# Kernel optimization log

Measured on AMD Instinct MI355X. Metric: run time of the kernel, lower is better.

Reference implementation:

```python
import jax, jax.numpy as jnp
import numpy as np

N_NODES = 10000
N_EDGES = 640000
D_IN, D_HID, D_OUT = 128, 128, 64


def setup_inputs() -> dict:
    key = jax.random.key(0)
    ks = jax.random.split(key, 12)
    inp = {
        "inputs": jax.random.normal(ks[0], (N_NODES, D_IN), dtype=jnp.float32),
        "W_self0": jax.random.normal(ks[1], (D_IN, D_HID), dtype=jnp.float32) / np.sqrt(D_IN),
        "W_neigh0": jax.random.normal(ks[2], (D_IN, D_HID), dtype=jnp.float32) / np.sqrt(D_IN),
        "b0": jnp.zeros((D_HID,), dtype=jnp.float32),
        "W_self1": jax.random.normal(ks[3], (D_HID, D_HID), dtype=jnp.float32) / np.sqrt(D_HID),
        "W_neigh1": jax.random.normal(ks[4], (D_HID, D_HID), dtype=jnp.float32) / np.sqrt(D_HID),
        "b1": jnp.zeros((D_HID,), dtype=jnp.float32),
        "W_self2": jax.random.normal(ks[5], (D_HID, D_OUT), dtype=jnp.float32) / np.sqrt(D_HID),
        "W_neigh2": jax.random.normal(ks[6], (D_HID, D_OUT), dtype=jnp.float32) / np.sqrt(D_HID),
        "b2": jnp.zeros((D_OUT,), dtype=jnp.float32),
        "edge_src": jax.random.randint(ks[7], (N_EDGES,), 0, N_NODES, dtype=jnp.int32),
        "edge_dst": jax.random.randint(ks[8], (N_EDGES,), 0, N_NODES, dtype=jnp.int32),
    }
    return inp


def _sage_conv(h, W_self, W_neigh, b, edge_src, edge_dst):
    # mean aggregation: mean of source-node features over incoming edges at dst
    gathered = h[edge_src]                                   # [E, d] irregular gather
    agg = jax.ops.segment_sum(gathered, edge_dst, num_segments=N_NODES)  # [N, d]
    deg = jax.ops.segment_sum(jnp.ones((edge_dst.shape[0],), h.dtype), edge_dst,
                              num_segments=N_NODES)          # [N]
    h_neigh = agg / jnp.maximum(deg, 1.0)[:, None]
    return h @ W_self + h_neigh @ W_neigh + b


def reference(inputs, W_self0, W_neigh0, b0, W_self1, W_neigh1, b1,
              W_self2, W_neigh2, b2, edge_src, edge_dst):
    # dropout p=0.0 -> identity
    h = _sage_conv(inputs, W_self0, W_neigh0, b0, edge_src, edge_dst)
    h = jax.nn.relu(h)
    h = _sage_conv(h, W_self1, W_neigh1, b1, edge_src, edge_dst)
    h = jax.nn.relu(h)
    h = _sage_conv(h, W_self2, W_neigh2, b2, edge_src, edge_dst)
    return h
```

## Files before the change

kernel.cpp:

```cpp
#include <hip/hip_runtime.h>


#define NN 10000
#define NE 640000
#define NBINS 313
#define NBLKA 250
#define CHUNK 2560
#define CAP 3072
#define SORT_CAP 4096

typedef __attribute__((ext_vector_type(8))) short s8v;
typedef __attribute__((ext_vector_type(4))) float f4v;

__device__ __forceinline__ ushort f2bf(float f) {
    unsigned u = __float_as_uint(f);
    return (ushort)((u + 0x7FFFu + ((u >> 16) & 1u)) >> 16);
}
__device__ __forceinline__ unsigned pack2(float a, float b) {
    return (unsigned)f2bf(a) | ((unsigned)f2bf(b) << 16);
}
__device__ __forceinline__ float bf_lo(unsigned u) { return __uint_as_float(u << 16); }
__device__ __forceinline__ float bf_hi(unsigned u) { return __uint_as_float(u & 0xFFFF0000u); }


__global__ void prep_k(const float* __restrict__ x, ushort* __restrict__ xb,
                       const float* __restrict__ Ws0, const float* __restrict__ Wn0,
                       const float* __restrict__ Ws1, const float* __restrict__ Wn1,
                       const float* __restrict__ Ws2, const float* __restrict__ Wn2,
                       ushort* __restrict__ wt, int* __restrict__ bincnt) {
    __shared__ ushort ps[128 * 128];
    int blk = blockIdx.x, tid = threadIdx.x;
    if (blk < 64) {
        const float4* xv = (const float4*)x;
        uint2* xo = (uint2*)xb;
        for (int i = tid; i < 5000; i += 256) {
            int idx = blk * 5000 + i;
            float4 v = xv[idx];
            xo[idx] = make_uint2(pack2(v.x, v.y), pack2(v.z, v.w));
        }
    } else if (blk < 70) {
        int m = blk - 64;
        const float* W = (m == 0) ? Ws0 : (m == 1) ? Wn0 : (m == 2) ? Ws1
                       : (m == 3) ? Wn1 : (m == 4) ? Ws2 : Wn2;
        int MC = (m < 4) ? 128 : 64;
        ushort* dst = wt + ((m < 4) ? m * 16384 : 65536 + (m - 4) * 8192);
        int tot = 128 * MC;
        for (int idx = tid; idx < tot; idx += 256) {
            int k = (MC == 128) ? (idx >> 7) : (idx >> 6);
            int n = (MC == 128) ? (idx & 127) : (idx & 63);
            ps[n * 128 + k] = f2bf(W[idx]);
        }
        __syncthreads();
        for (int idx = tid; idx < tot; idx += 256)
            dst[idx] = ps[idx];
    } else {
        for (int i = tid; i < NBINS; i += 256) bincnt[i] = 0;
    }
}


__device__ void scatter_body(const int* __restrict__ src, const int* __restrict__ dst,
                             int* __restrict__ bincnt, unsigned* __restrict__ tmp2,
                             int blk, int* smem) {
    int* h = smem;
    int* cur = smem + NBINS;
    int tid = threadIdx.x;
    for (int i = tid; i < NBINS; i += 256) h[i] = 0;
    __syncthreads();
    int base = blk * CHUNK;
    for (int i = tid; i < CHUNK; i += 256)
        atomicAdd(&h[dst[base + i] >> 5], 1);
    __syncthreads();
    for (int bin = tid; bin < NBINS; bin += 256) {
        int c = h[bin];
        int off = c ? atomicAdd(&bincnt[bin], c) : 0;
        cur[bin] = bin * CAP + off;
    }
    __syncthreads();
    for (int i = tid; i < CHUNK; i += 256) {
        int d = dst[base + i], s = src[base + i];
        int bin = d >> 5;
        int pos = atomicAdd(&cur[bin], 1);
        if (pos < bin * CAP + CAP)
            tmp2[pos] = ((unsigned)s << 5) | (unsigned)(d & 31);
    }
}

__device__ void dense0_body(const ushort* __restrict__ xb, const ushort* __restrict__ wt,
                            const float* __restrict__ b0,
                            float* __restrict__ hs, ushort* __restrict__ hn, int dblk) {
    int l = threadIdx.x & 63, w = threadIdx.x >> 6;
    int mloc = l & 15, quad = l >> 4;
    int row_base = dblk * 32 + (w & 1) * 16;
    int colh = w >> 1;
    int arow = row_base + mloc;
    int arow_c = (arow < NN) ? arow : (NN - 1);
    const ushort* wsT = wt;
    const ushort* wnT = wt + 16384;
    f4v accS[4], accN[4];
#pragma unroll
    for (int nt = 0; nt < 4; ++nt) { accS[nt] = (f4v){0,0,0,0}; accN[nt] = (f4v){0,0,0,0}; }
#pragma unroll
    for (int ks = 0; ks < 4; ++ks) {
        int kb = ks * 32 + quad * 8;
        s8v a = *(const s8v*)(xb + (size_t)arow_c * 128 + kb);
#pragma unroll
        for (int nt = 0; nt < 4; ++nt) {
            int n = colh * 64 + nt * 16 + mloc;
            s8v bs = *(const s8v*)(wsT + n * 128 + kb);
            s8v bn = *(const s8v*)(wnT + n * 128 + kb);
            accS[nt] = __builtin_amdgcn_mfma_f32_16x16x32_bf16(a, bs, accS[nt], 0, 0, 0);
            accN[nt] = __builtin_amdgcn_mfma_f32_16x16x32_bf16(a, bn, accN[nt], 0, 0, 0);
        }
    }
#pragma unroll
    for (int nt = 0; nt < 4; ++nt) {
        int col = colh * 64 + nt * 16 + mloc;
        float bv = b0[col];
#pragma unroll
        for (int r = 0; r < 4; ++r) {
            int row = row_base + quad * 4 + r;
            if (row < NN) {
                hs[(size_t)row * 128 + col] = accS[nt][r] + bv;
                hn[(size_t)row * 128 + col] = f2bf(accN[nt][r]);
            }
        }
    }
}

__global__ void scatdense_k(const int* __restrict__ esrc, const int* __restrict__ edst,
                            int* __restrict__ bincnt, unsigned* __restrict__ tmp2,
                            const ushort* __restrict__ xb, const ushort* __restrict__ wt,
                            const float* __restrict__ b0,
                            float* __restrict__ hs, ushort* __restrict__ hn) {
    __shared__ int smem[2 * NBINS];
    int blk = blockIdx.x;
    if (blk < NBLKA)
        scatter_body(esrc, edst, bincnt, tmp2, blk, smem);
    else
        dense0_body(xb, wt, b0, hs, hn, blk - NBLKA);
}


__global__ void sort_k(const unsigned* __restrict__ tmp2, const int* __restrict__ bincnt,
                       int* __restrict__ offs, int* __restrict__ ends,
                       int* __restrict__ ssrc) {
    __shared__ int stage[SORT_CAP];
    __shared__ int cnt32[32];
    __shared__ int cur32[32];
    int b = blockIdx.x, tid = threadIdx.x;
    int beg = b * CAP;
    int cnt = bincnt[b];
    if (cnt > CAP) cnt = CAP;
    if (tid < 32) cnt32[tid] = 0;
    __syncthreads();
    for (int i = tid; i < cnt; i += 256)
        atomicAdd(&cnt32[tmp2[beg + i] & 31], 1);
    __syncthreads();
    if (tid == 0) {
        int run = 0;
        for (int i = 0; i < 32; ++i) {
            int node = b * 32 + i;
            if (node < NN) { offs[node] = beg + run; ends[node] = beg + run + cnt32[i]; }
            cur32[i] = run;
            run += cnt32[i];
        }
    }
    __syncthreads();
    for (int i = tid; i < cnt; i += 256) {
        unsigned q = tmp2[beg + i];
        int pos = atomicAdd(&cur32[q & 31], 1);
        stage[pos] = (int)(q >> 5);
    }
    __syncthreads();
    for (int i = tid; i < cnt; i += 256)
        ssrc[beg + i] = stage[i];
}


template <int MOUT>
__global__ void agg_dense_k(const float* __restrict__ hs_in, const ushort* __restrict__ hn_in,
                            const int* __restrict__ offs, const int* __restrict__ ends,
                            const int* __restrict__ ssrc,
                            const ushort* __restrict__ wsT, const ushort* __restrict__ wnT,
                            const float* __restrict__ bias,
                            float* __restrict__ hs_out, ushort* __restrict__ hn_out) {
    __shared__ ushort hrow[16 * 136];
    int tid = threadIdx.x;
    int node_loc = tid >> 4, t = tid & 15;
    int node = blockIdx.x * 16 + node_loc;
    int beg = offs[node], end = ends[node];
    const uint4* hn4 = (const uint4*)hn_in;
    float a0 = 0, a1 = 0, a2 = 0, a3 = 0, a4 = 0, a5 = 0, a6 = 0, a7 = 0;
    int e = beg;
    for (; e + 8 <= end; e += 8) {
        int s0 = ssrc[e], s1 = ssrc[e + 1], s2 = ssrc[e + 2], s3 = ssrc[e + 3];
        int s4 = ssrc[e + 4], s5 = ssrc[e + 5], s6 = ssrc[e + 6], s7 = ssrc[e + 7];
        uint4 v0 = hn4[(size_t)s0 * 16 + t];
        uint4 v1 = hn4[(size_t)s1 * 16 + t];
        uint4 v2 = hn4[(size_t)s2 * 16 + t];
        uint4 v3 = hn4[(size_t)s3 * 16 + t];
        uint4 v4 = hn4[(size_t)s4 * 16 + t];
        uint4 v5 = hn4[(size_t)s5 * 16 + t];
        uint4 v6 = hn4[(size_t)s6 * 16 + t];
        uint4 v7 = hn4[(size_t)s7 * 16 + t];
        a0 += bf_lo(v0.x) + bf_lo(v1.x) + bf_lo(v2.x) + bf_lo(v3.x)
            + bf_lo(v4.x) + bf_lo(v5.x) + bf_lo(v6.x) + bf_lo(v7.x);
        a1 += bf_hi(v0.x) + bf_hi(v1.x) + bf_hi(v2.x) + bf_hi(v3.x)
            + bf_hi(v4.x) + bf_hi(v5.x) + bf_hi(v6.x) + bf_hi(v7.x);
        a2 += bf_lo(v0.y) + bf_lo(v1.y) + bf_lo(v2.y) + bf_lo(v3.y)
            + bf_lo(v4.y) + bf_lo(v5.y) + bf_lo(v6.y) + bf_lo(v7.y);
        a3 += bf_hi(v0.y) + bf_hi(v1.y) + bf_hi(v2.y) + bf_hi(v3.y)
            + bf_hi(v4.y) + bf_hi(v5.y) + bf_hi(v6.y) + bf_hi(v7.y);
        a4 += bf_lo(v0.z) + bf_lo(v1.z) + bf_lo(v2.z) + bf_lo(v3.z)
            + bf_lo(v4.z) + bf_lo(v5.z) + bf_lo(v6.z) + bf_lo(v7.z);
        a5 += bf_hi(v0.z) + bf_hi(v1.z) + bf_hi(v2.z) + bf_hi(v3.z)
            + bf_hi(v4.z) + bf_hi(v5.z) + bf_hi(v6.z) + bf_hi(v7.z);
        a6 += bf_lo(v0.w) + bf_lo(v1.w) + bf_lo(v2.w) + bf_lo(v3.w)
            + bf_lo(v4.w) + bf_lo(v5.w) + bf_lo(v6.w) + bf_lo(v7.w);
        a7 += bf_hi(v0.w) + bf_hi(v1.w) + bf_hi(v2.w) + bf_hi(v3.w)
            + bf_hi(v4.w) + bf_hi(v5.w) + bf_hi(v6.w) + bf_hi(v7.w);
    }
    for (; e < end; ++e) {
        uint4 v = hn4[(size_t)ssrc[e] * 16 + t];
        a0 += bf_lo(v.x); a1 += bf_hi(v.x); a2 += bf_lo(v.y); a3 += bf_hi(v.y);
        a4 += bf_lo(v.z); a5 += bf_hi(v.z); a6 += bf_lo(v.w); a7 += bf_hi(v.w);
    }
    int deg = end - beg;
    float sc = 1.0f / (float)(deg > 0 ? deg : 1);
    float4 h4a = ((const float4*)hs_in)[(size_t)node * 32 + 2 * t];
    float4 h4b = ((const float4*)hs_in)[(size_t)node * 32 + 2 * t + 1];
    float r0 = fmaxf(h4a.x + a0 * sc, 0.f), r1 = fmaxf(h4a.y + a1 * sc, 0.f);
    float r2 = fmaxf(h4a.z + a2 * sc, 0.f), r3 = fmaxf(h4a.w + a3 * sc, 0.f);
    float r4 = fmaxf(h4b.x + a4 * sc, 0.f), r5 = fmaxf(h4b.y + a5 * sc, 0.f);
    float r6 = fmaxf(h4b.z + a6 * sc, 0.f), r7 = fmaxf(h4b.w + a7 * sc, 0.f);
    *(uint4*)(hrow + node_loc * 136 + t * 8) =
        make_uint4(pack2(r0, r1), pack2(r2, r3), pack2(r4, r5), pack2(r6, r7));
    __syncthreads();

    int l = tid & 63, w = tid >> 6;
    int mloc = l & 15, quad = l >> 4;
    constexpr int NTPW = MOUT / 64;
    f4v accS[NTPW], accN[NTPW];
#pragma unroll
    for (int nt = 0; nt < NTPW; ++nt) { accS[nt] = (f4v){0,0,0,0}; accN[nt] = (f4v){0,0,0,0}; }
#pragma unroll
    for (int ks = 0; ks < 4; ++ks) {
        int kb = ks * 32 + quad * 8;
        s8v a = *(const s8v*)(hrow + mloc * 136 + kb);
#pragma unroll
        for (int nt = 0; nt < NTPW; ++nt) {
            int n = (w * NTPW + nt) * 16 + mloc;
            s8v bs = *(const s8v*)(wsT + n * 128 + kb);
            s8v bn = *(const s8v*)(wnT + n * 128 + kb);
            accS[nt] = __builtin_amdgcn_mfma_f32_16x16x32_bf16(a, bs, accS[nt], 0, 0, 0);
            accN[nt] = __builtin_amdgcn_mfma_f32_16x16x32_bf16(a, bn, accN[nt], 0, 0, 0);
        }
    }
#pragma unroll
    for (int nt = 0; nt < NTPW; ++nt) {
        int col = (w * NTPW + nt) * 16 + mloc;
        float bv = bias[col];
#pragma unroll
        for (int r = 0; r < 4; ++r) {
            int row = blockIdx.x * 16 + quad * 4 + r;
            hs_out[(size_t)row * MOUT + col] = accS[nt][r] + bv;
            hn_out[(size_t)row * MOUT + col] = f2bf(accN[nt][r]);
        }
    }
}


__global__ void agg_out_k(const float* __restrict__ hs_in, const ushort* __restrict__ hn_in,
                          const int* __restrict__ offs, const int* __restrict__ ends,
                          const int* __restrict__ ssrc, float* __restrict__ out) {
    int tid = threadIdx.x;
    int node = blockIdx.x * 32 + (tid >> 3);
    int t = tid & 7;
    if (node >= NN) return;
    int beg = offs[node], end = ends[node];
    const uint4* hn4 = (const uint4*)hn_in;
    float a0 = 0, a1 = 0, a2 = 0, a3 = 0, a4 = 0, a5 = 0, a6 = 0, a7 = 0;
    int e = beg;
    for (; e + 8 <= end; e += 8) {
        int s0 = ssrc[e], s1 = ssrc[e + 1], s2 = ssrc[e + 2], s3 = ssrc[e + 3];
        int s4 = ssrc[e + 4], s5 = ssrc[e + 5], s6 = ssrc[e + 6], s7 = ssrc[e + 7];
        uint4 v0 = hn4[(size_t)s0 * 8 + t];
        uint4 v1 = hn4[(size_t)s1 * 8 + t];
        uint4 v2 = hn4[(size_t)s2 * 8 + t];
        uint4 v3 = hn4[(size_t)s3 * 8 + t];
        uint4 v4 = hn4[(size_t)s4 * 8 + t];
        uint4 v5 = hn4[(size_t)s5 * 8 + t];
        uint4 v6 = hn4[(size_t)s6 * 8 + t];
        uint4 v7 = hn4[(size_t)s7 * 8 + t];
        a0 += bf_lo(v0.x) + bf_lo(v1.x) + bf_lo(v2.x) + bf_lo(v3.x)
            + bf_lo(v4.x) + bf_lo(v5.x) + bf_lo(v6.x) + bf_lo(v7.x);
        a1 += bf_hi(v0.x) + bf_hi(v1.x) + bf_hi(v2.x) + bf_hi(v3.x)
            + bf_hi(v4.x) + bf_hi(v5.x) + bf_hi(v6.x) + bf_hi(v7.x);
        a2 += bf_lo(v0.y) + bf_lo(v1.y) + bf_lo(v2.y) + bf_lo(v3.y)
            + bf_lo(v4.y) + bf_lo(v5.y) + bf_lo(v6.y) + bf_lo(v7.y);
        a3 += bf_hi(v0.y) + bf_hi(v1.y) + bf_hi(v2.y) + bf_hi(v3.y)
            + bf_hi(v4.y) + bf_hi(v5.y) + bf_hi(v6.y) + bf_hi(v7.y);
        a4 += bf_lo(v0.z) + bf_lo(v1.z) + bf_lo(v2.z) + bf_lo(v3.z)
            + bf_lo(v4.z) + bf_lo(v5.z) + bf_lo(v6.z) + bf_lo(v7.z);
        a5 += bf_hi(v0.z) + bf_hi(v1.z) + bf_hi(v2.z) + bf_hi(v3.z)
            + bf_hi(v4.z) + bf_hi(v5.z) + bf_hi(v6.z) + bf_hi(v7.z);
        a6 += bf_lo(v0.w) + bf_lo(v1.w) + bf_lo(v2.w) + bf_lo(v3.w)
            + bf_lo(v4.w) + bf_lo(v5.w) + bf_lo(v6.w) + bf_lo(v7.w);
        a7 += bf_hi(v0.w) + bf_hi(v1.w) + bf_hi(v2.w) + bf_hi(v3.w)
            + bf_hi(v4.w) + bf_hi(v5.w) + bf_hi(v6.w) + bf_hi(v7.w);
    }
    for (; e < end; ++e) {
        uint4 v = hn4[(size_t)ssrc[e] * 8 + t];
        a0 += bf_lo(v.x); a1 += bf_hi(v.x); a2 += bf_lo(v.y); a3 += bf_hi(v.y);
        a4 += bf_lo(v.z); a5 += bf_hi(v.z); a6 += bf_lo(v.w); a7 += bf_hi(v.w);
    }
    int deg = end - beg;
    float sc = 1.0f / (float)(deg > 0 ? deg : 1);
    float4 h4a = ((const float4*)hs_in)[(size_t)node * 16 + 2 * t];
    float4 h4b = ((const float4*)hs_in)[(size_t)node * 16 + 2 * t + 1];
    ((float4*)out)[(size_t)node * 16 + 2 * t] =
        make_float4(h4a.x + a0 * sc, h4a.y + a1 * sc, h4a.z + a2 * sc, h4a.w + a3 * sc);
    ((float4*)out)[(size_t)node * 16 + 2 * t + 1] =
        make_float4(h4b.x + a4 * sc, h4b.y + a5 * sc, h4b.z + a6 * sc, h4b.w + a7 * sc);
}


extern "C" void kernel_launch(void* const* d_in, const int* in_sizes, int n_in,
                              void* d_out, int out_size, void* d_ws, size_t ws_size,
                              hipStream_t stream) {
    const float* x   = (const float*)d_in[0];
    const float* Ws0 = (const float*)d_in[1];
    const float* Wn0 = (const float*)d_in[2];
    const float* b0  = (const float*)d_in[3];
    const float* Ws1 = (const float*)d_in[4];
    const float* Wn1 = (const float*)d_in[5];
    const float* b1  = (const float*)d_in[6];
    const float* Ws2 = (const float*)d_in[7];
    const float* Wn2 = (const float*)d_in[8];
    const float* b2  = (const float*)d_in[9];
    const int* esrc  = (const int*)d_in[10];
    const int* edst  = (const int*)d_in[11];
    float* out = (float*)d_out;

    float*  hsA = (float*)d_ws;
    float*  hsB = hsA + (size_t)NN * 128;
    ushort* hnA = (ushort*)(hsB + (size_t)NN * 128);
    ushort* hnB = hnA + (size_t)NN * 128;
    ushort* xb  = hnB + (size_t)NN * 128;
    ushort* wt  = xb + (size_t)NN * 128;
    unsigned* tmp2 = (unsigned*)(wt + 81920);
    int* ssrc = (int*)(tmp2 + (size_t)NBINS * CAP);
    int* offs = ssrc + (size_t)NBINS * CAP;
    int* ends = offs + NN;
    int* bincnt = ends + NN;

    prep_k<<<71, 256, 0, stream>>>(x, xb, Ws0, Wn0, Ws1, Wn1, Ws2, Wn2, wt, bincnt);
    scatdense_k<<<NBLKA + 313, 256, 0, stream>>>(esrc, edst, bincnt, tmp2,
                                                 xb, wt, b0, hsA, hnA);
    sort_k<<<NBINS, 256, 0, stream>>>(tmp2, bincnt, offs, ends, ssrc);
    agg_dense_k<128><<<NN / 16, 256, 0, stream>>>(hsA, hnA, offs, ends, ssrc,
                                                  wt + 32768, wt + 49152, b1, hsB, hnB);
    agg_dense_k<64><<<NN / 16, 256, 0, stream>>>(hsB, hnB, offs, ends, ssrc,
                                                 wt + 65536, wt + 73728, b2, hsA, hnA);
    agg_out_k<<<(NN + 31) / 32, 256, 0, stream>>>(hsA, hnA, offs, ends, ssrc, out);
}
```

Before: 169.2 us.

## Fuse input bf16 conversion into dense0 and move weight transposes into scatter kernel

Drops the separate pass that converts the node features to bf16; dense0 now reads fp32 rows directly and converts them in registers. The prep kernel shrinks to two blocks that only transpose the layer-0 weights, while the layer-1/2 weight transposes run as extra blocks of the scatter/dense kernel. The scatter pass now caches the packed edge words in shared memory so src/dst are read from global only once. This removes a full write and read of the bf16 feature buffer and shortens the prep launch, at the cost of a larger shared-memory footprint per block, which may lower occupancy, and of each dense0 block repeating the conversions.

Result: no change. 167.2 us (-1.2%).

```diff
diff --git a/kernel.cpp b/kernel.cpp
--- a/kernel.cpp
+++ b/kernel.cpp
@@ -22,39 +22,30 @@
 __device__ __forceinline__ float bf_lo(unsigned u) { return __uint_as_float(u << 16); }
 __device__ __forceinline__ float bf_hi(unsigned u) { return __uint_as_float(u & 0xFFFF0000u); }
 
-
-__global__ void prep_k(const float* __restrict__ x, ushort* __restrict__ xb,
-                       const float* __restrict__ Ws0, const float* __restrict__ Wn0,
-                       const float* __restrict__ Ws1, const float* __restrict__ Wn1,
-                       const float* __restrict__ Ws2, const float* __restrict__ Wn2,
+__device__ void wtrans_body(const float* __restrict__ W, ushort* __restrict__ dst,
+                            int MC, ushort* ps) {
+    int tid = threadIdx.x;
+    int tot = 128 * MC;
+    for (int idx = tid; idx < tot; idx += 256) {
+        int k = (MC == 128) ? (idx >> 7) : (idx >> 6);
+        int n = (MC == 128) ? (idx & 127) : (idx & 63);
+        ps[n * 128 + k] = f2bf(W[idx]);
+    }
+    __syncthreads();
+    for (int idx = tid; idx < tot; idx += 256)
+        dst[idx] = ps[idx];
+}
+
+
+__global__ void prep_k(const float* __restrict__ Ws0, const float* __restrict__ Wn0,
                        ushort* __restrict__ wt, int* __restrict__ bincnt) {
     __shared__ ushort ps[128 * 128];
     int blk = blockIdx.x, tid = threadIdx.x;
-    if (blk < 64) {
-        const float4* xv = (const float4*)x;
-        uint2* xo = (uint2*)xb;
-        for (int i = tid; i < 5000; i += 256) {
-            int idx = blk * 5000 + i;
-            float4 v = xv[idx];
-            xo[idx] = make_uint2(pack2(v.x, v.y), pack2(v.z, v.w));
-        }
-    } else if (blk < 70) {
-        int m = blk - 64;
-        const float* W = (m == 0) ? Ws0 : (m == 1) ? Wn0 : (m == 2) ? Ws1
-                       : (m == 3) ? Wn1 : (m == 4) ? Ws2 : Wn2;
-        int MC = (m < 4) ? 128 : 64;
-        ushort* dst = wt + ((m < 4) ? m * 16384 : 65536 + (m - 4) * 8192);
-        int tot = 128 * MC;
-        for (int idx = tid; idx < tot; idx += 256) {
-            int k = (MC == 128) ? (idx >> 7) : (idx >> 6);
-            int n = (MC == 128) ? (idx & 127) : (idx & 63);
-            ps[n * 128 + k] = f2bf(W[idx]);
-        }
-        __syncthreads();
-        for (int idx = tid; idx < tot; idx += 256)
-            dst[idx] = ps[idx];
+    if (blk == 0) {
+        for (int i = tid; i < NBINS; i += 256) bincnt[i] = 0;
+        wtrans_body(Ws0, wt, 128, ps);
     } else {
-        for (int i = tid; i < NBINS; i += 256) bincnt[i] = 0;
+        wtrans_body(Wn0, wt + 16384, 128, ps);
     }
 }
 
@@ -64,12 +55,17 @@
                              int blk, int* smem) {
     int* h = smem;
     int* cur = smem + NBINS;
+    unsigned* ec = (unsigned*)(smem + 2 * NBINS);
     int tid = threadIdx.x;
     for (int i = tid; i < NBINS; i += 256) h[i] = 0;
     __syncthreads();
     int base = blk * CHUNK;
-    for (int i = tid; i < CHUNK; i += 256)
-        atomicAdd(&h[dst[base + i] >> 5], 1);
+    for (int i = tid; i < CHUNK; i += 256) {
+        int d = dst[base + i], s = src[base + i];
+        int bin = d >> 5;
+        ec[i] = ((unsigned)bin << 19) | ((unsigned)s << 5) | (unsigned)(d & 31);
+        atomicAdd(&h[bin], 1);
+    }
     __syncthreads();
     for (int bin = tid; bin < NBINS; bin += 256) {
         int c = h[bin];
@@ -78,15 +74,15 @@
     }
     __syncthreads();
     for (int i = tid; i < CHUNK; i += 256) {
-        int d = dst[base + i], s = src[base + i];
-        int bin = d >> 5;
+        unsigned word = ec[i];
+        int bin = (int)(word >> 19);
         int pos = atomicAdd(&cur[bin], 1);
         if (pos < bin * CAP + CAP)
-            tmp2[pos] = ((unsigned)s << 5) | (unsigned)(d & 31);
-    }
-}
-
-__device__ void dense0_body(const ushort* __restrict__ xb, const ushort* __restrict__ wt,
+            tmp2[pos] = word & 0x7FFFFu;
+    }
+}
+
+__device__ void dense0_body(const float* __restrict__ x, const ushort* __restrict__ wt,
                             const float* __restrict__ b0,
                             float* __restrict__ hs, ushort* __restrict__ hn, int dblk) {
     int l = threadIdx.x & 63, w = threadIdx.x >> 6;
@@ -95,6 +91,7 @@
     int colh = w >> 1;
     int arow = row_base + mloc;
     int arow_c = (arow < NN) ? arow : (NN - 1);
+    const float4* xrow = (const float4*)(x + (size_t)arow_c * 128);
     const ushort* wsT = wt;
     const ushort* wnT = wt + 16384;
     f4v accS[4], accN[4];
@@ -103,7 +100,13 @@
 #pragma unroll
     for (int ks = 0; ks < 4; ++ks) {
         int kb = ks * 32 + quad * 8;
-        s8v a = *(const s8v*)(xb + (size_t)arow_c * 128 + kb);
+        float4 f0 = xrow[kb >> 2];
+        float4 f1 = xrow[(kb >> 2) + 1];
+        s8v a;
+        a[0] = (short)f2bf(f0.x); a[1] = (short)f2bf(f0.y);
+        a[2] = (short)f2bf(f0.z); a[3] = (short)f2bf(f0.w);
+        a[4] = (short)f2bf(f1.x); a[5] = (short)f2bf(f1.y);
+        a[6] = (short)f2bf(f1.z); a[7] = (short)f2bf(f1.w);
 #pragma unroll
         for (int nt = 0; nt < 4; ++nt) {
             int n = colh * 64 + nt * 16 + mloc;
@@ -130,15 +133,24 @@
 
 __global__ void scatdense_k(const int* __restrict__ esrc, const int* __restrict__ edst,
                             int* __restrict__ bincnt, unsigned* __restrict__ tmp2,
-                            const ushort* __restrict__ xb, const ushort* __restrict__ wt,
+                            const float* __restrict__ x, ushort* __restrict__ wt,
                             const float* __restrict__ b0,
-                            float* __restrict__ hs, ushort* __restrict__ hn) {
-    __shared__ int smem[2 * NBINS];
+                            float* __restrict__ hs, ushort* __restrict__ hn,
+                            const float* __restrict__ Ws1, const float* __restrict__ Wn1,
+                            const float* __restrict__ Ws2, const float* __restrict__ Wn2) {
+    __shared__ ushort ps[128 * 128];
     int blk = blockIdx.x;
-    if (blk < NBLKA)
-        scatter_body(esrc, edst, bincnt, tmp2, blk, smem);
-    else
-        dense0_body(xb, wt, b0, hs, hn, blk - NBLKA);
+    if (blk < NBLKA) {
+        scatter_body(esrc, edst, bincnt, tmp2, blk, (int*)ps);
+    } else if (blk < NBLKA + 313) {
+        dense0_body(x, wt, b0, hs, hn, blk - NBLKA);
+    } else {
+        int m = blk - NBLKA - 313;
+        const float* W = (m == 0) ? Ws1 : (m == 1) ? Wn1 : (m == 2) ? Ws2 : Wn2;
+        int MC = (m < 2) ? 128 : 64;
+        ushort* dst = wt + ((m < 2) ? 32768 + m * 16384 : 65536 + (m - 2) * 8192);
+        wtrans_body(W, dst, MC, ps);
+    }
 }
 
 
@@ -347,17 +359,17 @@
     float*  hsB = hsA + (size_t)NN * 128;
     ushort* hnA = (ushort*)(hsB + (size_t)NN * 128);
     ushort* hnB = hnA + (size_t)NN * 128;
-    ushort* xb  = hnB + (size_t)NN * 128;
-    ushort* wt  = xb + (size_t)NN * 128;
+    ushort* wt  = hnB + (size_t)NN * 128;
     unsigned* tmp2 = (unsigned*)(wt + 81920);
     int* ssrc = (int*)(tmp2 + (size_t)NBINS * CAP);
     int* offs = ssrc + (size_t)NBINS * CAP;
     int* ends = offs + NN;
     int* bincnt = ends + NN;
 
-    prep_k<<<71, 256, 0, stream>>>(x, xb, Ws0, Wn0, Ws1, Wn1, Ws2, Wn2, wt, bincnt);
-    scatdense_k<<<NBLKA + 313, 256, 0, stream>>>(esrc, edst, bincnt, tmp2,
-                                                 xb, wt, b0, hsA, hnA);
+    prep_k<<<2, 256, 0, stream>>>(Ws0, Wn0, wt, bincnt);
+    scatdense_k<<<NBLKA + 313 + 4, 256, 0, stream>>>(esrc, edst, bincnt, tmp2,
+                                                     x, wt, b0, hsA, hnA,
+                                                     Ws1, Wn1, Ws2, Wn2);
     sort_k<<<NBINS, 256, 0, stream>>>(tmp2, bincnt, offs, ends, ssrc);
     agg_dense_k<128><<<NN / 16, 256, 0, stream>>>(hsA, hnA, offs, ends, ssrc,
                                                   wt + 32768, wt + 49152, b1, hsB, hnB);
```
